# Performance work log

Measured on AMD Instinct MI355X. Metric: run time of the kernel, lower is better.

## Reference

```python
import jax, jax.numpy as jnp
import numpy as np

NUM_HEADS = 16
HEAD_DIM = 128  # 2048 / 16


def setup_inputs() -> dict:
    key = jax.random.key(0)
    ks = jax.random.split(key, 5)
    B, S, D = 2, 2048, 2048
    scale = 1.0 / np.sqrt(D)
    return {
        "x": jax.random.normal(ks[0], (B, S, D), dtype=jnp.float32),
        "Wq": jax.random.normal(ks[1], (D, D), dtype=jnp.float32) * scale,
        "Wk": jax.random.normal(ks[2], (D, D), dtype=jnp.float32) * scale,
        "Wv": jax.random.normal(ks[3], (D, D), dtype=jnp.float32) * scale,
        "Wo": jax.random.normal(ks[4], (D, D), dtype=jnp.float32) * scale,
    }


def reference(x, Wq, Wk, Wv, Wo):
    B, S, D = x.shape
    H, Hd = NUM_HEADS, HEAD_DIM
    # nn.Linear(bias=False): y = x @ W.T
    q = (x @ Wq.T).reshape(B, S, H, Hd).transpose(0, 2, 1, 3)  # [B,H,S,Hd]
    k = (x @ Wk.T).reshape(B, S, H, Hd).transpose(0, 2, 1, 3)
    v = (x @ Wv.T).reshape(B, S, H, Hd).transpose(0, 2, 1, 3)
    scores = jnp.einsum("bhqd,bhkd->bhqk", q, k) / jnp.sqrt(jnp.float32(Hd))
    attn = jax.nn.softmax(scores, axis=-1)  # dropout p=0 (eval) -> identity
    out = jnp.einsum("bhqk,bhkd->bhqd", attn, v)  # [B,H,S,Hd]
    out = out.transpose(0, 2, 1, 3).reshape(B, S, D)
    out = out @ Wo.T
    return out
```

## Files before the change

### kernel.cpp

```cpp
#include <hip/hip_runtime.h>
#include <math.h>
#include <stdint.h>


#define DDIM 2048
#define SEQ  2048
#define NH   16
#define HD   128

typedef __attribute__((ext_vector_type(4))) float f32x4;
typedef __attribute__((ext_vector_type(16))) float f32x16;
typedef __attribute__((ext_vector_type(8))) __bf16 bf16x8;
typedef __attribute__((ext_vector_type(4))) unsigned int u32x4;
typedef __attribute__((ext_vector_type(2))) unsigned int u32x2;

#define MFMA_B16(a, b, c) __builtin_amdgcn_mfma_f32_16x16x32_bf16((a), (b), (c), 0, 0, 0)
#define MFMA32(a, b, c) __builtin_amdgcn_mfma_f32_32x32x16_bf16((a), (b), (c), 0, 0, 0)

__device__ __forceinline__ void async16(const void* g, void* l) {
  __builtin_amdgcn_global_load_lds(
      (const __attribute__((address_space(1))) unsigned int*)g,
      (__attribute__((address_space(3))) unsigned int*)l, 16, 0, 0);
}

__device__ __forceinline__ unsigned short f2bf(float f) {
  unsigned u = __builtin_bit_cast(unsigned, f);
  u += 0x7fffu + ((u >> 16) & 1u);
  return (unsigned short)(u >> 16);
}

__device__ __forceinline__ bf16x8 ldfrag(const unsigned short* p) {
  return __builtin_bit_cast(bf16x8, *(const u32x4*)p);
}

__device__ __forceinline__ void cvt_body(const float* __restrict__ s,
                                         unsigned short* __restrict__ d, int i) {
  const f32x4* sp = (const f32x4*)s;
  f32x4 a = sp[2 * i], b = sp[2 * i + 1];
  u32x4 o;
  o.x = ((unsigned)f2bf(a.y) << 16) | f2bf(a.x);
  o.y = ((unsigned)f2bf(a.w) << 16) | f2bf(a.z);
  o.z = ((unsigned)f2bf(b.y) << 16) | f2bf(b.x);
  o.w = ((unsigned)f2bf(b.w) << 16) | f2bf(b.z);
  ((u32x4*)d)[i] = o;
}

__global__ __launch_bounds__(256) void cvt_bf16_kernel(const float* __restrict__ s,
                                                       unsigned short* __restrict__ d) {
  cvt_body(s, d, blockIdx.x * 256 + threadIdx.x);
}

__global__ __launch_bounds__(256) void cvt_all_kernel(const float* __restrict__ x,
                                                      const float* __restrict__ wq,
                                                      const float* __restrict__ wk,
                                                      const float* __restrict__ wv,
                                                      const float* __restrict__ wo,
                                                      unsigned short* __restrict__ xb,
                                                      unsigned short* __restrict__ wqkv,
                                                      unsigned short* __restrict__ wob) {
  const int b = blockIdx.x;
  if (b < 4096) {
    cvt_body(x, xb, b * 256 + threadIdx.x);
  } else if (b < 10240) {
    const int wi = (b - 4096) >> 11, lb = (b - 4096) & 2047;
    const float* s = (wi == 0) ? wq : (wi == 1) ? wk : wv;
    cvt_body(s, wqkv + (size_t)wi * 4194304u, lb * 256 + threadIdx.x);
  } else {
    cvt_body(wo, wob, (b - 10240) * 256 + threadIdx.x);
  }
}

template <int MODE>
__global__ __launch_bounds__(256) void gemm32(const unsigned short* __restrict__ A,
                                              const unsigned short* __restrict__ B,
                                              unsigned short* __restrict__ Oqk,
                                              unsigned short* __restrict__ Ovt,
                                              float* __restrict__ Cf, float alpha_q) {
  __shared__ unsigned short As[128 * 64];
  __shared__ unsigned short Bs[128 * 64];
  const int tid = threadIdx.x;
  const int lane = tid & 63, w = tid >> 6;
  const int l32 = lane & 31, half = lane >> 5;
  const int wm = (w >> 1) * 64, wn = (w & 1) * 64;
  const int bm = blockIdx.y * 128, bn = blockIdx.x * 128;

  f32x16 acc[2][2];
#pragma unroll
  for (int i = 0; i < 2; ++i)
#pragma unroll
    for (int j = 0; j < 2; ++j)
#pragma unroll
      for (int e = 0; e < 16; ++e) acc[i][j][e] = 0.f;

  const unsigned short* pa[4];
  const unsigned short* pbb[4];
  {
#pragma unroll
    for (int j = 0; j < 4; ++j) {
      const int row = j * 32 + (tid >> 3);
      const int cg = (tid & 7) ^ (row & 7) ^ ((row >> 3) & 7);
      pa[j] = A + (size_t)(bm + row) * DDIM + cg * 8;
      pbb[j] = B + (size_t)(bn + row) * DDIM + cg * 8;
    }
  }

  const int fr = (l32 & 7) ^ (l32 >> 3);

  for (int kt = 0; kt < DDIM / 64; ++kt) {
    __syncthreads();
#pragma unroll
    for (int j = 0; j < 4; ++j) {
      async16(pa[j], &As[(j * 256 + tid) * 8]);
      pa[j] += 64;
      async16(pbb[j], &Bs[(j * 256 + tid) * 8]);
      pbb[j] += 64;
    }
    __syncthreads();
#pragma unroll
    for (int ks = 0; ks < 4; ++ks) {
      const int ph = ks * 2 + half;
      const int sl0 = (ph ^ fr) * 8;
      const int sl1 = (ph ^ fr ^ 4) * 8;
      bf16x8 af0 = ldfrag(&As[(wm + l32) * 64 + sl0]);
      bf16x8 af1 = ldfrag(&As[(wm + 32 + l32) * 64 + sl1]);
      bf16x8 bf0 = ldfrag(&Bs[(wn + l32) * 64 + sl0]);
      bf16x8 bf1 = ldfrag(&Bs[(wn + 32 + l32) * 64 + sl1]);
      acc[0][0] = MFMA32(af0, bf0, acc[0][0]);
      acc[0][1] = MFMA32(af0, bf1, acc[0][1]);
      acc[1][0] = MFMA32(af1, bf0, acc[1][0]);
      acc[1][1] = MFMA32(af1, bf1, acc[1][1]);
    }
  }

  const int seg = (MODE == 0) ? (bn >> 11) : 0;
  const int bnl = bn & 2047;
  const float alpha = (MODE == 0 && seg == 0) ? alpha_q : 1.0f;
#pragma unroll
  for (int i = 0; i < 2; ++i) {
#pragma unroll
    for (int j = 0; j < 2; ++j) {
#pragma unroll
      for (int rg = 0; rg < 4; ++rg) {
        const int m0 = bm + wm + i * 32 + rg * 8 + half * 4;
        const float v0 = acc[i][j][rg * 4 + 0] * alpha;
        const float v1 = acc[i][j][rg * 4 + 1] * alpha;
        const float v2 = acc[i][j][rg * 4 + 2] * alpha;
        const float v3 = acc[i][j][rg * 4 + 3] * alpha;
        if (MODE == 1) {
          const int n = bn + wn + j * 32 + l32;
          Cf[(size_t)(m0 + 0) * DDIM + n] = v0;
          Cf[(size_t)(m0 + 1) * DDIM + n] = v1;
          Cf[(size_t)(m0 + 2) * DDIM + n] = v2;
          Cf[(size_t)(m0 + 3) * DDIM + n] = v3;
        } else {
          const int n = bnl + wn + j * 32 + l32;
          if (seg < 2) {
            unsigned short* O = Oqk + (size_t)seg * (4096u * 2048u);
            O[(size_t)(m0 + 0) * DDIM + n] = f2bf(v0);
            O[(size_t)(m0 + 1) * DDIM + n] = f2bf(v1);
            O[(size_t)(m0 + 2) * DDIM + n] = f2bf(v2);
            O[(size_t)(m0 + 3) * DDIM + n] = f2bf(v3);
          } else {
            const int bb = m0 >> 11, s0 = m0 & 2047;
            const int hh = n >> 7, dd = n & 127;
            u32x2 st;
            st.x = ((unsigned)f2bf(v1) << 16) | f2bf(v0);
            st.y = ((unsigned)f2bf(v3) << 16) | f2bf(v2);
            *(u32x2*)&Ovt[((size_t)((bb * NH + hh) * HD + dd)) * SEQ + s0] = st;
          }
        }
      }
    }
  }
}

__global__ __launch_bounds__(512) void attn_kernel(const unsigned short* __restrict__ qb,
                                                   const unsigned short* __restrict__ kb,
                                                   const unsigned short* __restrict__ vtb,
                                                   unsigned short* __restrict__ ab) {
  __shared__ unsigned short Ks[64 * 128];
  __shared__ unsigned short Vts[128 * 64];
  __shared__ unsigned short Pw[8 * 16 * 40];
  const int tid = threadIdx.x;
  const int w = tid >> 6, lane = tid & 63;
  const int quad = lane >> 4, l16 = lane & 15;
  const int qt = blockIdx.x, bh = blockIdx.y;
  const int b = bh >> 4, h = bh & 15;
  const int qrow = qt * 128 + w * 16 + l16;

  const unsigned short* qp = qb + ((size_t)(b * SEQ + qrow)) * DDIM + h * HD;
  bf16x8 qf[4];
#pragma unroll
  for (int ks = 0; ks < 4; ++ks) qf[ks] = ldfrag(qp + ks * 32 + quad * 8);

  f32x4 ot[8];
#pragma unroll
  for (int i = 0; i < 8; i++) ot[i] = f32x4{0.f, 0.f, 0.f, 0.f};
  float sumacc = 0.f;

  const unsigned short* kp[2];
  const unsigned short* vp[2];
  {
    const size_t kbase = ((size_t)(b * SEQ)) * DDIM + h * HD;
    const size_t vbase = ((size_t)((b * NH + h) * HD)) * SEQ;
#pragma unroll
    for (int j = 0; j < 2; ++j) {
      const int key = j * 32 + (tid >> 4), cgk = (tid & 15) ^ (key & 15);
      kp[j] = kb + kbase + (size_t)key * DDIM + cgk * 8;
      const int dd = j * 64 + (tid >> 3), cgv = (tid & 7) ^ (dd & 7);
      vp[j] = vtb + vbase + (size_t)dd * SEQ + cgv * 8;
    }
  }
  unsigned short* pw = &Pw[w * 640];

  for (int kt = 0; kt < SEQ / 64; ++kt) {
    __syncthreads();
#pragma unroll
    for (int j = 0; j < 2; ++j) {
      async16(kp[j], &Ks[(j * 512 + tid) * 8]);
      kp[j] += (size_t)64 * DDIM;
      async16(vp[j], &Vts[(j * 512 + tid) * 8]);
      vp[j] += 64;
    }
    __syncthreads();
    f32x4 s[4];
#pragma unroll
    for (int t = 0; t < 4; ++t) s[t] = f32x4{0.f, 0.f, 0.f, 0.f};
#pragma unroll
    for (int ks = 0; ks < 4; ++ks) {
      const int sl = ((ks * 4 + quad) ^ l16) * 8;
#pragma unroll
      for (int t = 0; t < 4; ++t) {
        bf16x8 a = ldfrag(&Ks[(t * 16 + l16) * 128 + sl]);
        s[t] = MFMA_B16(a, qf[ks], s[t]);
      }
    }
    f32x4 p[4];
#pragma unroll
    for (int t = 0; t < 4; ++t) {
      p[t].x = __builtin_amdgcn_exp2f(s[t].x);
      p[t].y = __builtin_amdgcn_exp2f(s[t].y);
      p[t].z = __builtin_amdgcn_exp2f(s[t].z);
      p[t].w = __builtin_amdgcn_exp2f(s[t].w);
      sumacc += (p[t].x + p[t].y) + (p[t].z + p[t].w);
    }
    bf16x8 pb0, pb1;
    {
      u32x2 w0, w1;
      w0.x = ((unsigned)f2bf(p[0].y) << 16) | f2bf(p[0].x);
      w0.y = ((unsigned)f2bf(p[0].w) << 16) | f2bf(p[0].z);
      w1.x = ((unsigned)f2bf(p[1].y) << 16) | f2bf(p[1].x);
      w1.y = ((unsigned)f2bf(p[1].w) << 16) | f2bf(p[1].z);
      *(u32x2*)&pw[l16 * 40 + quad * 4] = w0;
      *(u32x2*)&pw[l16 * 40 + 16 + quad * 4] = w1;
      asm volatile("s_waitcnt lgkmcnt(0)" ::: "memory");
      pb0 = ldfrag(&pw[l16 * 40 + quad * 8]);
      w0.x = ((unsigned)f2bf(p[2].y) << 16) | f2bf(p[2].x);
      w0.y = ((unsigned)f2bf(p[2].w) << 16) | f2bf(p[2].z);
      w1.x = ((unsigned)f2bf(p[3].y) << 16) | f2bf(p[3].x);
      w1.y = ((unsigned)f2bf(p[3].w) << 16) | f2bf(p[3].z);
      *(u32x2*)&pw[l16 * 40 + quad * 4] = w0;
      *(u32x2*)&pw[l16 * 40 + 16 + quad * 4] = w1;
      asm volatile("s_waitcnt lgkmcnt(0)" ::: "memory");
      pb1 = ldfrag(&pw[l16 * 40 + quad * 8]);
    }
#pragma unroll
    for (int mt = 0; mt < 8; ++mt) {
      bf16x8 vf0 = ldfrag(&Vts[(mt * 16 + l16) * 64 + (quad ^ (l16 & 7)) * 8]);
      ot[mt] = MFMA_B16(vf0, pb0, ot[mt]);
      bf16x8 vf1 = ldfrag(&Vts[(mt * 16 + l16) * 64 + ((4 + quad) ^ (l16 & 7)) * 8]);
      ot[mt] = MFMA_B16(vf1, pb1, ot[mt]);
    }
  }
  float total = sumacc;
  total += __shfl_xor(total, 16);
  total += __shfl_xor(total, 32);
  const float inv = 1.0f / total;
  unsigned short* op = ab + ((size_t)(b * SEQ + qrow)) * DDIM + h * HD;
#pragma unroll
  for (int mt = 0; mt < 8; ++mt) {
    f32x4 v = ot[mt] * inv;
    u32x2 st;
    st.x = ((unsigned)f2bf(v.y) << 16) | f2bf(v.x);
    st.y = ((unsigned)f2bf(v.w) << 16) | f2bf(v.z);
    *(u32x2*)&op[mt * 16 + quad * 4] = st;
  }
}

extern "C" void kernel_launch(void* const* d_in, const int* in_sizes, int n_in,
                              void* d_out, int out_size, void* d_ws, size_t ws_size,
                              hipStream_t stream) {
  (void)in_sizes; (void)n_in; (void)out_size;
  const float* x = (const float*)d_in[0];
  const float* Wq = (const float*)d_in[1];
  const float* Wk = (const float*)d_in[2];
  const float* Wv = (const float*)d_in[3];
  const float* Wo = (const float*)d_in[4];

  char* ws = (char*)d_ws;
  unsigned short* xb = (unsigned short*)(ws);
  unsigned short* wqkv = (unsigned short*)(ws + 16777216);
  unsigned short* qb = (unsigned short*)(ws + 41943040);
  unsigned short* kb = (unsigned short*)(ws + 58720256);
  unsigned short* vtb = (unsigned short*)(ws + 75497472);
  const bool big = ws_size >= 100663296ull;
  unsigned short* wob = big ? (unsigned short*)(ws + 92274688) : wqkv;

  const float alpha_q = 1.44269504088896341f / sqrtf(128.0f);

  if (big) {
    cvt_all_kernel<<<dim3(12288), 256, 0, stream>>>(x, Wq, Wk, Wv, Wo, xb, wqkv, wob);
    gemm32<0><<<dim3(48, 32), 256, 0, stream>>>(xb, wqkv, qb, vtb, nullptr, alpha_q);
  } else {
    cvt_all_kernel<<<dim3(10240), 256, 0, stream>>>(x, Wq, Wk, Wv, Wo, xb, wqkv, wob);
    gemm32<0><<<dim3(48, 32), 256, 0, stream>>>(xb, wqkv, qb, vtb, nullptr, alpha_q);
    cvt_bf16_kernel<<<dim3(2048), 256, 0, stream>>>(Wo, wob);
  }

  attn_kernel<<<dim3(16, 32), 512, 0, stream>>>(qb, kb, vtb, xb);

  gemm32<1><<<dim3(16, 32), 256, 0, stream>>>(xb, wob, nullptr, nullptr, (float*)d_out,
                                              1.0f);
}
```

Before: 368.8 us.

## Split-K output projection with atomics and XCD-aware attention block mapping

```diff
diff --git a/kernel.cpp b/kernel.cpp
--- a/kernel.cpp
+++ b/kernel.cpp
@@ -57,7 +57,9 @@
                                                       const float* __restrict__ wo,
                                                       unsigned short* __restrict__ xb,
                                                       unsigned short* __restrict__ wqkv,
-                                                      unsigned short* __restrict__ wob) {
+                                                      unsigned short* __restrict__ wob,
+                                                      float* __restrict__ dout,
+                                                      int has_wo) {
   const int b = blockIdx.x;
   if (b < 4096) {
     cvt_body(x, xb, b * 256 + threadIdx.x);
@@ -65,8 +67,17 @@
     const int wi = (b - 4096) >> 11, lb = (b - 4096) & 2047;
     const float* s = (wi == 0) ? wq : (wi == 1) ? wk : wv;
     cvt_body(s, wqkv + (size_t)wi * 4194304u, lb * 256 + threadIdx.x);
+  } else if (has_wo && b < 12288) {
+    cvt_body(wo, wob, (b - 10240) * 256 + threadIdx.x);
   } else {
-    cvt_body(wo, wob, (b - 10240) * 256 + threadIdx.x);
+    const int zb = b - (has_wo ? 12288 : 10240);
+    f32x4* zp = (f32x4*)dout;
+    const int i = zb * 256 + threadIdx.x;
+    const f32x4 z = {0.f, 0.f, 0.f, 0.f};
+    zp[i] = z;
+    zp[i + 524288] = z;
+    zp[i + 1048576] = z;
+    zp[i + 1572864] = z;
   }
 }
 
@@ -83,6 +94,7 @@
   const int l32 = lane & 31, half = lane >> 5;
   const int wm = (w >> 1) * 64, wn = (w & 1) * 64;
   const int bm = blockIdx.y * 128, bn = blockIdx.x * 128;
+  const int nkt = (MODE == 1) ? 16 : 32;
 
   f32x16 acc[2][2];
 #pragma unroll
@@ -95,18 +107,19 @@
   const unsigned short* pa[4];
   const unsigned short* pbb[4];
   {
+    const size_t k0 = (size_t)blockIdx.z * (nkt * 64);
 #pragma unroll
     for (int j = 0; j < 4; ++j) {
       const int row = j * 32 + (tid >> 3);
       const int cg = (tid & 7) ^ (row & 7) ^ ((row >> 3) & 7);
-      pa[j] = A + (size_t)(bm + row) * DDIM + cg * 8;
-      pbb[j] = B + (size_t)(bn + row) * DDIM + cg * 8;
+      pa[j] = A + (size_t)(bm + row) * DDIM + k0 + cg * 8;
+      pbb[j] = B + (size_t)(bn + row) * DDIM + k0 + cg * 8;
     }
   }
 
   const int fr = (l32 & 7) ^ (l32 >> 3);
 
-  for (int kt = 0; kt < DDIM / 64; ++kt) {
+  for (int kt = 0; kt < nkt; ++kt) {
     __syncthreads();
 #pragma unroll
     for (int j = 0; j < 4; ++j) {
@@ -148,10 +161,10 @@
         const float v3 = acc[i][j][rg * 4 + 3] * alpha;
         if (MODE == 1) {
           const int n = bn + wn + j * 32 + l32;
-          Cf[(size_t)(m0 + 0) * DDIM + n] = v0;
-          Cf[(size_t)(m0 + 1) * DDIM + n] = v1;
-          Cf[(size_t)(m0 + 2) * DDIM + n] = v2;
-          Cf[(size_t)(m0 + 3) * DDIM + n] = v3;
+          unsafeAtomicAdd(&Cf[(size_t)(m0 + 0) * DDIM + n], v0);
+          unsafeAtomicAdd(&Cf[(size_t)(m0 + 1) * DDIM + n], v1);
+          unsafeAtomicAdd(&Cf[(size_t)(m0 + 2) * DDIM + n], v2);
+          unsafeAtomicAdd(&Cf[(size_t)(m0 + 3) * DDIM + n], v3);
         } else {
           const int n = bnl + wn + j * 32 + l32;
           if (seg < 2) {
@@ -184,7 +197,10 @@
   const int tid = threadIdx.x;
   const int w = tid >> 6, lane = tid & 63;
   const int quad = lane >> 4, l16 = lane & 15;
-  const int qt = blockIdx.x, bh = blockIdx.y;
+  const int bid = blockIdx.y * 16 + blockIdx.x;
+  const int xcd = bid & 7, slot = bid >> 3;
+  const int bh = xcd * 4 + (slot >> 4);
+  const int qt = slot & 15;
   const int b = bh >> 4, h = bh & 15;
   const int qrow = qt * 128 + w * 16 + l16;
 
@@ -305,20 +321,22 @@
   unsigned short* vtb = (unsigned short*)(ws + 75497472);
   const bool big = ws_size >= 100663296ull;
   unsigned short* wob = big ? (unsigned short*)(ws + 92274688) : wqkv;
+  float* dout = (float*)d_out;
 
   const float alpha_q = 1.44269504088896341f / sqrtf(128.0f);
 
   if (big) {
-    cvt_all_kernel<<<dim3(12288), 256, 0, stream>>>(x, Wq, Wk, Wv, Wo, xb, wqkv, wob);
+    cvt_all_kernel<<<dim3(14336), 256, 0, stream>>>(x, Wq, Wk, Wv, Wo, xb, wqkv, wob,
+                                                    dout, 1);
     gemm32<0><<<dim3(48, 32), 256, 0, stream>>>(xb, wqkv, qb, vtb, nullptr, alpha_q);
   } else {
-    cvt_all_kernel<<<dim3(10240), 256, 0, stream>>>(x, Wq, Wk, Wv, Wo, xb, wqkv, wob);
+    cvt_all_kernel<<<dim3(12288), 256, 0, stream>>>(x, Wq, Wk, Wv, Wo, xb, wqkv, wob,
+                                                    dout, 0);
     gemm32<0><<<dim3(48, 32), 256, 0, stream>>>(xb, wqkv, qb, vtb, nullptr, alpha_q);
     cvt_bf16_kernel<<<dim3(2048), 256, 0, stream>>>(Wo, wob);
   }
 
   attn_kernel<<<dim3(16, 32), 512, 0, stream>>>(qb, kb, vtb, xb);
 
-  gemm32<1><<<dim3(16, 32), 256, 0, stream>>>(xb, wob, nullptr, nullptr, (float*)d_out,
-                                              1.0f);
-}
+  gemm32<1><<<dim3(16, 32, 2), 256, 0, stream>>>(xb, wob, nullptr, nullptr, dout, 1.0f);
+}
```

Result: slower. 408.1 us (+10.7%).
